# Kernel optimization log

Hardware: AMD Instinct MI355X
Metric: run time of the kernel (lower is better)

## Reference

```python
import jax, jax.numpy as jnp
import numpy as np
import math

N = 512
XDIM = 256
EDIM = 128
N_HEAD = 8
DF = XDIM // N_HEAD


def _linear(x, W, b):
    # torch nn.Linear: y = x @ W.T + b, W is [out, in]
    return x @ W.T + b


def setup_inputs() -> dict:
    key = jax.random.key(0)
    ks = jax.random.split(key, 20)
    s = 0.02
    inp = {
        "x": jax.random.normal(ks[0], (N, XDIM), jnp.float32),
        "e": jax.random.normal(ks[1], (N, N, EDIM), jnp.float32),
        "adj": jax.random.uniform(ks[2], (N, N), jnp.float32),
        "Wq": jax.random.normal(ks[3], (XDIM, XDIM), jnp.float32) * s,
        "bq": jnp.zeros((XDIM,), jnp.float32),
        "Wk": jax.random.normal(ks[4], (XDIM, XDIM), jnp.float32) * s,
        "bk": jnp.zeros((XDIM,), jnp.float32),
        "Wv": jax.random.normal(ks[5], (XDIM, XDIM), jnp.float32) * s,
        "bv": jnp.zeros((XDIM,), jnp.float32),
        "Wem": jax.random.normal(ks[6], (XDIM, EDIM), jnp.float32) * s,
        "bem": jnp.zeros((XDIM,), jnp.float32),
        "Wea": jax.random.normal(ks[7], (XDIM, EDIM), jnp.float32) * s,
        "bea": jnp.zeros((XDIM,), jnp.float32),
        "Wxo": jax.random.normal(ks[8], (XDIM, XDIM), jnp.float32) * s,
        "bxo": jnp.zeros((XDIM,), jnp.float32),
        "Weo": jax.random.normal(ks[9], (EDIM, XDIM), jnp.float32) * s,
        "beo": jnp.zeros((EDIM,), jnp.float32),
    }
    return inp


def reference(x, e, adj, Wq, bq, Wk, bk, Wv, bv, Wem, bem, Wea, bea, Wxo, bxo, Weo, beo):
    n = x.shape[0]
    Q = _linear(x, Wq, bq).reshape(n, N_HEAD, DF)  # [N, H, df]
    K = _linear(x, Wk, bk).reshape(n, N_HEAD, DF)
    # elementwise (non-dot) score: [N, N, H, df]
    Y = (Q[:, None, :, :] * K[None, :, :, :]) / math.sqrt(DF)
    E1 = _linear(e, Wem, bem).reshape(n, n, N_HEAD, DF)
    E2 = _linear(e, Wea, bea).reshape(n, n, N_HEAD, DF)
    Y = Y * (E1 + 1.0) + E2
    newE = _linear(Y.reshape(n, n, XDIM), Weo, beo)  # [N, N, edim]
    attn = jax.nn.softmax(Y, axis=1)  # softmax over key-node axis (dim=1)
    V = _linear(x, Wv, bv).reshape(n, N_HEAD, DF)
    weighted_V = (attn * V[None, :, :, :]).sum(axis=1)  # [N, H, df]
    newX = _linear(weighted_V.reshape(n, XDIM), Wxo, bxo)
    return (newX, newE)
```

## Files before the change

### kernel.cpp

```cpp
#include <hip/hip_runtime.h>
#include <math.h>

#define NN 512
#define XD 256
#define ED 128
#define JC 32
#define NCHUNK (NN/JC)
#define SE_STRIDE 136
#define SY_STRIDE 264

typedef __attribute__((ext_vector_type(8))) short s8v;
typedef __attribute__((ext_vector_type(4))) float f4v;

__device__ __forceinline__ short f2bf(float f) {
    union { float f; unsigned u; } v; v.f = f;
    unsigned r = (v.u + 0x7FFFu + ((v.u >> 16) & 1u)) >> 16;
    return (short)r;
}
__device__ __forceinline__ s8v load8_bf(const float* __restrict__ p) {
    const float4* p4 = (const float4*)p;
    float4 a = p4[0], b = p4[1];
    s8v r;
    r[0]=f2bf(a.x); r[1]=f2bf(a.y); r[2]=f2bf(a.z); r[3]=f2bf(a.w);
    r[4]=f2bf(b.x); r[5]=f2bf(b.y); r[6]=f2bf(b.z); r[7]=f2bf(b.w);
    return r;
}
__device__ __forceinline__ unsigned cvt_pk_bf16(float lo, float hi) {
    unsigned r;
    asm("v_cvt_pk_bf16_f32 %0, %1, %2" : "=v"(r) : "v"(lo), "v"(hi));
    return r;
}

__global__ void wconv_kernel(const float* __restrict__ Wem, const float* __restrict__ Wea,
                             const float* __restrict__ Weo,
                             short* __restrict__ Wem_bf, short* __restrict__ Wea_bf,
                             short* __restrict__ Weo_bf) {
    const int f = blockIdx.x * 256 + threadIdx.x;
    const int lane = f & 63;
    const int quad = lane >> 4;
    const int l16  = lane & 15;
    if (blockIdx.y < 2) {
        const float* src = blockIdx.y == 0 ? Wem : Wea;
        short* dst = blockIdx.y == 0 ? Wem_bf : Wea_bf;
        const int cb = f >> 8;
        const int ks = (f >> 6) & 3;
        *(s8v*)(dst + (size_t)f * 8) =
            load8_bf(src + (size_t)(cb*16 + l16)*ED + ks*32 + quad*8);
    } else {
        const int ob = f >> 9;
        const int ks = (f >> 6) & 7;
        *(s8v*)(Weo_bf + (size_t)f * 8) =
            load8_bf(Weo + (size_t)(ob*16 + l16)*XD + ks*32 + quad*8);
    }
}

__global__ void qkv_kernel(const float* __restrict__ x,
                           const float* __restrict__ Wq, const float* __restrict__ bq,
                           const float* __restrict__ Wk, const float* __restrict__ bk,
                           const float* __restrict__ Wv, const float* __restrict__ bv,
                           float* __restrict__ out) {
    const int i = blockIdx.x, which = blockIdx.y, t = threadIdx.x;
    __shared__ float sx[XD];
    sx[t] = x[i*XD + t];
    __syncthreads();
    const float* W = which==0 ? Wq : (which==1 ? Wk : Wv);
    const float* b = which==0 ? bq : (which==1 ? bk : bv);
    const float4* W4 = (const float4*)(W + (size_t)t*XD);
    const float4* x4 = (const float4*)sx;
    float acc = 0.f;
    #pragma unroll 8
    for (int k4 = 0; k4 < XD/4; ++k4) {
        float4 w = W4[k4]; float4 xv = x4[k4];
        acc += w.x*xv.x + w.y*xv.y + w.z*xv.z + w.w*xv.w;
    }
    acc += b[t];
    if (which == 0) acc *= 0.17677669529663688f;
    out[((size_t)which*NN + i)*XD + t] = acc;
}

__global__ __launch_bounds__(512, 4) void pass1_kernel(
    const float* __restrict__ e,
    const float* __restrict__ Qs, const float* __restrict__ Km, const float* __restrict__ Vm,
    const short* __restrict__ Wem_bf, const float* __restrict__ bem,
    const short* __restrict__ Wea_bf, const float* __restrict__ bea,
    const short* __restrict__ Weo_bf, const float* __restrict__ beo,
    float* __restrict__ outE,
    float* __restrict__ Pm, float* __restrict__ Pl, float* __restrict__ Pa)
{
    __shared__ __align__(16) short sE[JC*SE_STRIDE];
    __shared__ __align__(16) short sY[JC*SY_STRIDE];

    const int ch = blockIdx.x;
    const int i  = blockIdx.y;
    const int t = threadIdx.x;
    const int wave = t >> 6;
    const int lane = t & 63;
    const int quad = (lane >> 4) & 3;
    const int l16 = lane & 15;
    const int wn0 = wave * 32;

    float q_l[2], bm1[2], bea_l[2];
    #pragma unroll
    for (int nt = 0; nt < 2; ++nt) {
        const int c = wn0 + nt*16 + l16;
        q_l[nt]   = Qs[i*XD + c];
        bm1[nt]   = bem[c] + 1.0f;
        bea_l[nt] = bea[c];
    }
    const int oo = wave*16 + l16;
    const float beo_l = beo[oo];

    const s8v* W1p = (const s8v*)(Wem_bf + ((size_t)wave*8*64 + lane)*8);
    const s8v* W2p = (const s8v*)(Wea_bf + ((size_t)wave*8*64 + lane)*8);
    const s8v* W3p = (const s8v*)(Weo_bf + ((size_t)wave*8*64 + lane)*8);

    {
        const int sj = t >> 4;
        const int sk = (t & 15) * 8;
        const float4* p4 = (const float4*)(e + ((size_t)i*NN + (size_t)(ch*JC + sj))*ED + sk);
        float4 a = p4[0], b = p4[1];
        unsigned u0 = cvt_pk_bf16(a.x, a.y), u1 = cvt_pk_bf16(a.z, a.w);
        unsigned u2 = cvt_pk_bf16(b.x, b.y), u3 = cvt_pk_bf16(b.z, b.w);
        int4 pk; pk.x=(int)u0; pk.y=(int)u1; pk.z=(int)u2; pk.w=(int)u3;
        *(int4*)(&sE[sj*SE_STRIDE + sk]) = pk;
    }

    const float* Kb = Km + ((size_t)(ch*JC) + quad*4)*XD + wn0 + l16;
    const float* Vb = Vm + ((size_t)(ch*JC) + quad*4)*XD + wn0 + l16;
    float kv[2][2][4];
    #pragma unroll
    for (int mt = 0; mt < 2; ++mt)
        #pragma unroll
        for (int nt = 0; nt < 2; ++nt)
            #pragma unroll
            for (int r = 0; r < 4; ++r)
                kv[mt][nt][r] = Kb[(mt*16 + r)*XD + nt*16];

    __syncthreads();

    f4v acc1[2][2], acc2[2][2];
    #pragma unroll
    for (int mt = 0; mt < 2; ++mt)
        #pragma unroll
        for (int nt = 0; nt < 2; ++nt) {
            f4v z = {0.f, 0.f, 0.f, 0.f};
            acc1[mt][nt] = z; acc2[mt][nt] = z;
        }
    #pragma unroll
    for (int ks = 0; ks < 4; ++ks) {
        s8v a0 = *(const s8v*)(&sE[(     l16)*SE_STRIDE + ks*32 + quad*8]);
        s8v a1 = *(const s8v*)(&sE[(16 + l16)*SE_STRIDE + ks*32 + quad*8]);
        #pragma unroll
        for (int nt = 0; nt < 2; ++nt) {
            s8v b1 = W1p[(nt*4 + ks)*64];
            s8v b2 = W2p[(nt*4 + ks)*64];
            acc1[0][nt] = __builtin_amdgcn_mfma_f32_16x16x32_bf16(a0, b1, acc1[0][nt], 0, 0, 0);
            acc1[1][nt] = __builtin_amdgcn_mfma_f32_16x16x32_bf16(a1, b1, acc1[1][nt], 0, 0, 0);
            acc2[0][nt] = __builtin_amdgcn_mfma_f32_16x16x32_bf16(a0, b2, acc2[0][nt], 0, 0, 0);
            acc2[1][nt] = __builtin_amdgcn_mfma_f32_16x16x32_bf16(a1, b2, acc2[1][nt], 0, 0, 0);
        }
    }

    float y[2][2][4];
    #pragma unroll
    for (int mt = 0; mt < 2; ++mt)
        #pragma unroll
        for (int nt = 0; nt < 2; ++nt)
            #pragma unroll
            for (int r = 0; r < 4; ++r) {
                float e1 = acc1[mt][nt][r] + bm1[nt];
                float e2 = acc2[mt][nt][r] + bea_l[nt];
                y[mt][nt][r] = q_l[nt]*kv[mt][nt][r]*e1 + e2;
            }

    #pragma unroll
    for (int mt = 0; mt < 2; ++mt)
        #pragma unroll
        for (int nt = 0; nt < 2; ++nt) {
            unsigned p01 = cvt_pk_bf16(y[mt][nt][0], y[mt][nt][1]);
            unsigned p23 = cvt_pk_bf16(y[mt][nt][2], y[mt][nt][3]);
            short* b = &sY[(mt*16 + quad*4)*SY_STRIDE + wn0 + nt*16 + l16];
            b[0]            = (short)p01;
            b[SY_STRIDE]    = (short)(p01 >> 16);
            b[2*SY_STRIDE]  = (short)p23;
            b[3*SY_STRIDE]  = (short)(p23 >> 16);
        }

    float Mc[2], Lc[2], Ac[2];
    {
        float vv[2][2][4];
        #pragma unroll
        for (int mt = 0; mt < 2; ++mt)
            #pragma unroll
            for (int nt = 0; nt < 2; ++nt)
                #pragma unroll
                for (int r = 0; r < 4; ++r)
                    vv[mt][nt][r] = Vb[(mt*16 + r)*XD + nt*16];
        #pragma unroll
        for (int nt = 0; nt < 2; ++nt) {
            float m = fmaxf(
                fmaxf(fmaxf(y[0][nt][0], y[0][nt][1]), fmaxf(y[0][nt][2], y[0][nt][3])),
                fmaxf(fmaxf(y[1][nt][0], y[1][nt][1]), fmaxf(y[1][nt][2], y[1][nt][3])));
            m = fmaxf(m, __shfl_xor(m, 16));
            m = fmaxf(m, __shfl_xor(m, 32));
            float l = 0.f, a = 0.f;
            #pragma unroll
            for (int mt = 0; mt < 2; ++mt)
                #pragma unroll
                for (int r = 0; r < 4; ++r) {
                    float p = __expf(y[mt][nt][r] - m);
                    l += p;
                    a += p * vv[mt][nt][r];
                }
            l += __shfl_xor(l, 16); l += __shfl_xor(l, 32);
            a += __shfl_xor(a, 16); a += __shfl_xor(a, 32);
            Mc[nt] = m; Lc[nt] = l; Ac[nt] = a;
        }
    }

    __syncthreads();

    f4v acc3[2];
    {
        f4v z = {0.f, 0.f, 0.f, 0.f};
        acc3[0] = z; acc3[1] = z;
    }
    #pragma unroll
    for (int ks = 0; ks < 8; ++ks) {
        s8v b3 = W3p[ks*64];
        s8v a0 = *(const s8v*)(&sY[(     l16)*SY_STRIDE + ks*32 + quad*8]);
        s8v a1 = *(const s8v*)(&sY[(16 + l16)*SY_STRIDE + ks*32 + quad*8]);
        acc3[0] = __builtin_amdgcn_mfma_f32_16x16x32_bf16(a0, b3, acc3[0], 0, 0, 0);
        acc3[1] = __builtin_amdgcn_mfma_f32_16x16x32_bf16(a1, b3, acc3[1], 0, 0, 0);
    }
    #pragma unroll
    for (int mt = 0; mt < 2; ++mt)
        #pragma unroll
        for (int r = 0; r < 4; ++r) {
            const int jg = ch*JC + mt*16 + quad*4 + r;
            outE[((size_t)i*NN + jg)*ED + oo] = acc3[mt][r] + beo_l;
        }

    if (quad == 0) {
        #pragma unroll
        for (int nt = 0; nt < 2; ++nt) {
            const size_t pb = ((size_t)i*NCHUNK + ch)*256 + wn0 + nt*16 + l16;
            Pm[pb] = Mc[nt];
            Pl[pb] = Lc[nt];
            Pa[pb] = Ac[nt];
        }
    }
}

__global__ void pass2_kernel(const float* __restrict__ Pm, const float* __restrict__ Pl,
                             const float* __restrict__ Pa,
                             const float* __restrict__ Wxo, const float* __restrict__ bxo,
                             float* __restrict__ outX) {
    const int i = blockIdx.x, t = threadIdx.x;
    float mloc[NCHUNK];
    float M = -INFINITY;
    #pragma unroll
    for (int ch = 0; ch < NCHUNK; ++ch) {
        mloc[ch] = Pm[((size_t)i*NCHUNK + ch)*256 + t];
        M = fmaxf(M, mloc[ch]);
    }
    float L = 0.f, A = 0.f;
    #pragma unroll
    for (int ch = 0; ch < NCHUNK; ++ch) {
        const size_t pb = ((size_t)i*NCHUNK + ch)*256 + t;
        float s = __expf(mloc[ch] - M);
        L += Pl[pb]*s;
        A += Pa[pb]*s;
    }
    __shared__ float sv[XD];
    sv[t] = A / L;
    __syncthreads();
    const float4* W4 = (const float4*)(Wxo + (size_t)t*XD);
    const float4* v4 = (const float4*)sv;
    float acc = 0.f;
    #pragma unroll 8
    for (int k4 = 0; k4 < XD/4; ++k4) {
        float4 w = W4[k4]; float4 v = v4[k4];
        acc += w.x*v.x + w.y*v.y + w.z*v.z + w.w*v.w;
    }
    outX[(size_t)i*XD + t] = acc + bxo[t];
}

extern "C" void kernel_launch(void* const* d_in, const int* in_sizes, int n_in,
                              void* d_out, int out_size, void* d_ws, size_t ws_size,
                              hipStream_t stream) {
    const float* x   = (const float*)d_in[0];
    const float* e   = (const float*)d_in[1];
    const float* Wq  = (const float*)d_in[3];
    const float* bq  = (const float*)d_in[4];
    const float* Wk  = (const float*)d_in[5];
    const float* bk  = (const float*)d_in[6];
    const float* Wv  = (const float*)d_in[7];
    const float* bv  = (const float*)d_in[8];
    const float* Wem = (const float*)d_in[9];
    const float* bem = (const float*)d_in[10];
    const float* Wea = (const float*)d_in[11];
    const float* bea = (const float*)d_in[12];
    const float* Wxo = (const float*)d_in[13];
    const float* bxo = (const float*)d_in[14];
    const float* Weo = (const float*)d_in[15];
    const float* beo = (const float*)d_in[16];

    float* ws = (float*)d_ws;
    float* Qs = ws;
    float* Km = ws + (size_t)NN*XD;
    float* Vm = ws + (size_t)2*NN*XD;
    float* Pm = ws + (size_t)3*NN*XD;
    float* Pl = Pm + (size_t)NN*NCHUNK*XD;
    float* Pa = Pl + (size_t)NN*NCHUNK*XD;
    short* Wem_bf = (short*)(Pa + (size_t)NN*NCHUNK*XD);
    short* Wea_bf = Wem_bf + (size_t)XD*ED;
    short* Weo_bf = Wea_bf + (size_t)XD*ED;

    float* outX = (float*)d_out;
    float* outE = outX + (size_t)NN*XD;

    wconv_kernel<<<dim3(16, 3), 256, 0, stream>>>(Wem, Wea, Weo, Wem_bf, Wea_bf, Weo_bf);
    qkv_kernel<<<dim3(NN, 3), 256, 0, stream>>>(x, Wq, bq, Wk, bk, Wv, bv, ws);
    pass1_kernel<<<dim3(NCHUNK, NN), 512, 0, stream>>>(e, Qs, Km, Vm,
                                                       Wem_bf, bem, Wea_bf, bea,
                                                       Weo_bf, beo, outE, Pm, Pl, Pa);
    pass2_kernel<<<NN, 256, 0, stream>>>(Pm, Pl, Pa, Wxo, bxo, outX);
}
```

Baseline: 384.8 us.

## Double pass1 key-chunk to 64 rows and preload weight fragments into registers

Raises the per-block key chunk from 32 to 64 rows, so each block processes four 16-row M tiles and reuses each weight fragment across twice as many MFMAs. The Wem, Wea and Weo bf16 fragments are now loaded into registers once, up front, instead of being re-read inside the MFMA loops. The V loads are issued earlier, and the launch-bounds occupancy hint rises from 4 to 6. This halves the grid and the number of partial softmax records, but raises register pressure and LDS per block, which may spill or reduce real occupancy.

```diff
diff --git a/kernel.cpp b/kernel.cpp
--- a/kernel.cpp
+++ b/kernel.cpp
@@ -4,7 +4,7 @@
 #define NN 512
 #define XD 256
 #define ED 128
-#define JC 32
+#define JC 64
 #define NCHUNK (NN/JC)
 #define SE_STRIDE 136
 #define SY_STRIDE 264
@@ -78,7 +78,7 @@
     out[((size_t)which*NN + i)*XD + t] = acc;
 }
 
-__global__ __launch_bounds__(512, 4) void pass1_kernel(
+__global__ __launch_bounds__(512, 6) void pass1_kernel(
     const float* __restrict__ e,
     const float* __restrict__ Qs, const float* __restrict__ Km, const float* __restrict__ Vm,
     const short* __restrict__ Wem_bf, const float* __restrict__ bem,
@@ -114,22 +114,34 @@
     const s8v* W2p = (const s8v*)(Wea_bf + ((size_t)wave*8*64 + lane)*8);
     const s8v* W3p = (const s8v*)(Weo_bf + ((size_t)wave*8*64 + lane)*8);
 
+    s8v W1f[2][4], W2f[2][4];
+    #pragma unroll
+    for (int nt = 0; nt < 2; ++nt)
+        #pragma unroll
+        for (int ks = 0; ks < 4; ++ks) {
+            W1f[nt][ks] = W1p[(nt*4 + ks)*64];
+            W2f[nt][ks] = W2p[(nt*4 + ks)*64];
+        }
+
     {
-        const int sj = t >> 4;
-        const int sk = (t & 15) * 8;
+        const int sj = t >> 3;
+        const int sk = (t & 7) * 16;
         const float4* p4 = (const float4*)(e + ((size_t)i*NN + (size_t)(ch*JC + sj))*ED + sk);
-        float4 a = p4[0], b = p4[1];
-        unsigned u0 = cvt_pk_bf16(a.x, a.y), u1 = cvt_pk_bf16(a.z, a.w);
-        unsigned u2 = cvt_pk_bf16(b.x, b.y), u3 = cvt_pk_bf16(b.z, b.w);
-        int4 pk; pk.x=(int)u0; pk.y=(int)u1; pk.z=(int)u2; pk.w=(int)u3;
-        *(int4*)(&sE[sj*SE_STRIDE + sk]) = pk;
+        float4 a = p4[0], b = p4[1], c = p4[2], d = p4[3];
+        int4 pk0, pk1;
+        pk0.x=(int)cvt_pk_bf16(a.x,a.y); pk0.y=(int)cvt_pk_bf16(a.z,a.w);
+        pk0.z=(int)cvt_pk_bf16(b.x,b.y); pk0.w=(int)cvt_pk_bf16(b.z,b.w);
+        pk1.x=(int)cvt_pk_bf16(c.x,c.y); pk1.y=(int)cvt_pk_bf16(c.z,c.w);
+        pk1.z=(int)cvt_pk_bf16(d.x,d.y); pk1.w=(int)cvt_pk_bf16(d.z,d.w);
+        *(int4*)(&sE[sj*SE_STRIDE + sk])     = pk0;
+        *(int4*)(&sE[sj*SE_STRIDE + sk + 8]) = pk1;
     }
 
     const float* Kb = Km + ((size_t)(ch*JC) + quad*4)*XD + wn0 + l16;
     const float* Vb = Vm + ((size_t)(ch*JC) + quad*4)*XD + wn0 + l16;
-    float kv[2][2][4];
-    #pragma unroll
-    for (int mt = 0; mt < 2; ++mt)
+    float kv[4][2][4];
+    #pragma unroll
+    for (int mt = 0; mt < 4; ++mt)
         #pragma unroll
         for (int nt = 0; nt < 2; ++nt)
             #pragma unroll
@@ -138,9 +150,9 @@
 
     __syncthreads();
 
-    f4v acc1[2][2], acc2[2][2];
-    #pragma unroll
-    for (int mt = 0; mt < 2; ++mt)
+    f4v acc1[4][2], acc2[4][2];
+    #pragma unroll
+    for (int mt = 0; mt < 4; ++mt)
         #pragma unroll
         for (int nt = 0; nt < 2; ++nt) {
             f4v z = {0.f, 0.f, 0.f, 0.f};
@@ -148,22 +160,25 @@
         }
     #pragma unroll
     for (int ks = 0; ks < 4; ++ks) {
-        s8v a0 = *(const s8v*)(&sE[(     l16)*SE_STRIDE + ks*32 + quad*8]);
-        s8v a1 = *(const s8v*)(&sE[(16 + l16)*SE_STRIDE + ks*32 + quad*8]);
+        s8v a[4];
+        #pragma unroll
+        for (int mt = 0; mt < 4; ++mt)
+            a[mt] = *(const s8v*)(&sE[(mt*16 + l16)*SE_STRIDE + ks*32 + quad*8]);
         #pragma unroll
         for (int nt = 0; nt < 2; ++nt) {
-            s8v b1 = W1p[(nt*4 + ks)*64];
-            s8v b2 = W2p[(nt*4 + ks)*64];
-            acc1[0][nt] = __builtin_amdgcn_mfma_f32_16x16x32_bf16(a0, b1, acc1[0][nt], 0, 0, 0);
-            acc1[1][nt] = __builtin_amdgcn_mfma_f32_16x16x32_bf16(a1, b1, acc1[1][nt], 0, 0, 0);
-            acc2[0][nt] = __builtin_amdgcn_mfma_f32_16x16x32_bf16(a0, b2, acc2[0][nt], 0, 0, 0);
-            acc2[1][nt] = __builtin_amdgcn_mfma_f32_16x16x32_bf16(a1, b2, acc2[1][nt], 0, 0, 0);
-        }
-    }
-
-    float y[2][2][4];
-    #pragma unroll
-    for (int mt = 0; mt < 2; ++mt)
+            s8v b1 = W1f[nt][ks];
+            s8v b2 = W2f[nt][ks];
+            #pragma unroll
+            for (int mt = 0; mt < 4; ++mt) {
+                acc1[mt][nt] = __builtin_amdgcn_mfma_f32_16x16x32_bf16(a[mt], b1, acc1[mt][nt], 0, 0, 0);
+                acc2[mt][nt] = __builtin_amdgcn_mfma_f32_16x16x32_bf16(a[mt], b2, acc2[mt][nt], 0, 0, 0);
+            }
+        }
+    }
+
+    float y[4][2][4];
+    #pragma unroll
+    for (int mt = 0; mt < 4; ++mt)
         #pragma unroll
         for (int nt = 0; nt < 2; ++nt)
             #pragma unroll
@@ -173,8 +188,21 @@
                 y[mt][nt][r] = q_l[nt]*kv[mt][nt][r]*e1 + e2;
             }
 
-    #pragma unroll
-    for (int mt = 0; mt < 2; ++mt)
+    float vv[4][2][4];
+    #pragma unroll
+    for (int mt = 0; mt < 4; ++mt)
+        #pragma unroll
+        for (int nt = 0; nt < 2; ++nt)
+            #pragma unroll
+            for (int r = 0; r < 4; ++r)
+                vv[mt][nt][r] = Vb[(mt*16 + r)*XD + nt*16];
+    s8v W3f[8];
+    #pragma unroll
+    for (int ks = 0; ks < 8; ++ks)
+        W3f[ks] = W3p[ks*64];
+
+    #pragma unroll
+    for (int mt = 0; mt < 4; ++mt)
         #pragma unroll
         for (int nt = 0; nt < 2; ++nt) {
             unsigned p01 = cvt_pk_bf16(y[mt][nt][0], y[mt][nt][1]);
@@ -187,54 +215,49 @@
         }
 
     float Mc[2], Lc[2], Ac[2];
-    {
-        float vv[2][2][4];
-        #pragma unroll
-        for (int mt = 0; mt < 2; ++mt)
-            #pragma unroll
-            for (int nt = 0; nt < 2; ++nt)
-                #pragma unroll
-                for (int r = 0; r < 4; ++r)
-                    vv[mt][nt][r] = Vb[(mt*16 + r)*XD + nt*16];
-        #pragma unroll
-        for (int nt = 0; nt < 2; ++nt) {
-            float m = fmaxf(
-                fmaxf(fmaxf(y[0][nt][0], y[0][nt][1]), fmaxf(y[0][nt][2], y[0][nt][3])),
-                fmaxf(fmaxf(y[1][nt][0], y[1][nt][1]), fmaxf(y[1][nt][2], y[1][nt][3])));
-            m = fmaxf(m, __shfl_xor(m, 16));
-            m = fmaxf(m, __shfl_xor(m, 32));
-            float l = 0.f, a = 0.f;
-            #pragma unroll
-            for (int mt = 0; mt < 2; ++mt)
-                #pragma unroll
-                for (int r = 0; r < 4; ++r) {
-                    float p = __expf(y[mt][nt][r] - m);
-                    l += p;
-                    a += p * vv[mt][nt][r];
-                }
-            l += __shfl_xor(l, 16); l += __shfl_xor(l, 32);
-            a += __shfl_xor(a, 16); a += __shfl_xor(a, 32);
-            Mc[nt] = m; Lc[nt] = l; Ac[nt] = a;
-        }
+    #pragma unroll
+    for (int nt = 0; nt < 2; ++nt) {
+        float m = -INFINITY;
+        #pragma unroll
+        for (int mt = 0; mt < 4; ++mt)
+            #pragma unroll
+            for (int r = 0; r < 4; ++r)
+                m = fmaxf(m, y[mt][nt][r]);
+        m = fmaxf(m, __shfl_xor(m, 16));
+        m = fmaxf(m, __shfl_xor(m, 32));
+        float l = 0.f, a = 0.f;
+        #pragma unroll
+        for (int mt = 0; mt < 4; ++mt)
+            #pragma unroll
+            for (int r = 0; r < 4; ++r) {
+                float p = __expf(y[mt][nt][r] - m);
+                l += p;
+                a += p * vv[mt][nt][r];
+            }
+        l += __shfl_xor(l, 16); l += __shfl_xor(l, 32);
+        a += __shfl_xor(a, 16); a += __shfl_xor(a, 32);
+        Mc[nt] = m; Lc[nt] = l; Ac[nt] = a;
     }
 
     __syncthreads();
 
-    f4v acc3[2];
-    {
+    f4v acc3[4];
+    #pragma unroll
+    for (int mt = 0; mt < 4; ++mt) {
         f4v z = {0.f, 0.f, 0.f, 0.f};
-        acc3[0] = z; acc3[1] = z;
+        acc3[mt] = z;
     }
     #pragma unroll
     for (int ks = 0; ks < 8; ++ks) {
-        s8v b3 = W3p[ks*64];
-        s8v a0 = *(const s8v*)(&sY[(     l16)*SY_STRIDE + ks*32 + quad*8]);
-        s8v a1 = *(const s8v*)(&sY[(16 + l16)*SY_STRIDE + ks*32 + quad*8]);
-        acc3[0] = __builtin_amdgcn_mfma_f32_16x16x32_bf16(a0, b3, acc3[0], 0, 0, 0);
-        acc3[1] = __builtin_amdgcn_mfma_f32_16x16x32_bf16(a1, b3, acc3[1], 0, 0, 0);
-    }
-    #pragma unroll
-    for (int mt = 0; mt < 2; ++mt)
+        s8v b3 = W3f[ks];
+        #pragma unroll
+        for (int mt = 0; mt < 4; ++mt) {
+            s8v a = *(const s8v*)(&sY[(mt*16 + l16)*SY_STRIDE + ks*32 + quad*8]);
+            acc3[mt] = __builtin_amdgcn_mfma_f32_16x16x32_bf16(a, b3, acc3[mt], 0, 0, 0);
+        }
+    }
+    #pragma unroll
+    for (int mt = 0; mt < 4; ++mt)
         #pragma unroll
         for (int r = 0; r < 4; ++r) {
             const int jg = ch*JC + mt*16 + quad*4 + r;
```

Measured after the change: 1.080 ms. 2.81x slower.
